# Kernel tuning notes

Hardware: AMD Instinct MI355X
Metric: run time of the kernel (lower is better)

Reference implementation:

```python
import jax, jax.numpy as jnp
import numpy as np

D_MODEL = 1024
MAX_ELEMENTS = 128


def setup_inputs() -> dict:
    key = jax.random.key(0)
    ks = jax.random.split(key, 12)
    B, S = 256, 128
    d, dq = D_MODEL, D_MODEL // 4
    inp = {
        "element_types": jax.random.randint(ks[0], (B, S), 0, 5, dtype=jnp.int64 if jax.config.jax_enable_x64 else jnp.int32),
        "element_indices": jax.random.randint(ks[1], (B, S), 0, MAX_ELEMENTS, dtype=jnp.int64 if jax.config.jax_enable_x64 else jnp.int32),
        "style_vectors": jax.random.normal(ks[2], (B, 5), dtype=jnp.float32),
        "page_captions": jax.random.normal(ks[3], (B, 768), dtype=jnp.float32),
        # learned parameters (torch Linear stored as [in, out] so y = x @ W + b)
        "type_emb": jax.random.normal(ks[4], (5, d), dtype=jnp.float32) * 0.02,
        "pos_emb": jax.random.normal(ks[5], (MAX_ELEMENTS, d), dtype=jnp.float32) * 0.02,
        "style_w1": jax.random.normal(ks[6], (5, dq), dtype=jnp.float32) * 0.02,
        "style_b1": jnp.zeros((dq,), dtype=jnp.float32),
        "style_w2": jax.random.normal(ks[7], (dq, d), dtype=jnp.float32) * 0.02,
        "style_b2": jnp.zeros((d,), dtype=jnp.float32),
        "text_w": jax.random.normal(ks[8], (768, d), dtype=jnp.float32) * 0.02,
        "text_b": jnp.zeros((d,), dtype=jnp.float32),
        "final_pos_emb": jax.random.normal(ks[9], (MAX_ELEMENTS, d), dtype=jnp.float32) * 0.02,
    }
    return inp


def reference(element_types, element_indices, style_vectors, page_captions,
              type_emb, pos_emb, style_w1, style_b1, style_w2, style_b2,
              text_w, text_b, final_pos_emb):
    B, S = element_types.shape
    # table gathers: [B, S, d]
    emb = type_emb[element_types] + pos_emb[element_indices]
    # per-batch style/text embeds computed ONCE (the torch loop recomputes them per step)
    style_embed = jnp.maximum(style_vectors @ style_w1 + style_b1, 0.0) @ style_w2 + style_b2  # [B, d]
    page_embed = page_captions @ text_w + text_b  # [B, d]
    # loop over i with mask (types[:, i] == 1) == broadcast masked add
    mask1 = (element_types == 1)[:, :, None]  # [B, S, 1]
    emb = emb + mask1 * (style_embed + page_embed)[:, None, :]
    # final positional encoding over positions 0..S-1
    emb = emb + final_pos_emb[:S][None, :, :]
    padding_mask = element_types == 0
    return emb, padding_mask
```

## Files before the change

kernel.cpp:

```cpp
#include <hip/hip_runtime.h>

#define D      1024
#define SEQ    128
#define BATCH  256
#define DQ     256
#define TEXTC  768

__global__ __launch_bounds__(256) void prep_kernel(
    const float* __restrict__ style_vectors,
    const float* __restrict__ page_captions,
    const float* __restrict__ style_w1,
    const float* __restrict__ style_b1,
    const float* __restrict__ style_b2,
    const float* __restrict__ text_b,
    float* __restrict__ act,
    float* __restrict__ comb)
{
    int i = blockIdx.x * 256 + threadIdx.x;
    int b = i >> 10;
    int k = i & 1023;
    float a;
    if (k < DQ) {
        float h = style_b1[k];
#pragma unroll
        for (int j = 0; j < 5; ++j)
            h = fmaf(style_vectors[b * 5 + j], style_w1[j * DQ + k], h);
        a = fmaxf(h, 0.0f);
    } else {
        a = page_captions[b * TEXTC + (k - DQ)];
    }
    act[i]  = a;
    comb[i] = style_b2[k] + text_b[k];
}

__global__ __launch_bounds__(256) void gemm_kernel(
    const float* __restrict__ act,
    const float* __restrict__ style_w2,
    const float* __restrict__ text_w,
    float* __restrict__ comb)
{
    __shared__ float As[16][64];
    __shared__ float Bs[16][64];

    const int m0  = blockIdx.x * 64;
    const int n0  = blockIdx.y * 64;
    const int k0  = blockIdx.z * 256;
    const int tid = threadIdx.x;
    const int tm  = tid >> 4;
    const int tn  = tid & 15;

    float acc[4][4] = {};

    for (int kc = 0; kc < 256; kc += 16) {
        {
            int m  = tid >> 2;
            int kq = tid & 3;
            float4 av = *(const float4*)&act[(m0 + m) * D + k0 + kc + kq * 4];
            As[kq * 4 + 0][m] = av.x;
            As[kq * 4 + 1][m] = av.y;
            As[kq * 4 + 2][m] = av.z;
            As[kq * 4 + 3][m] = av.w;
        }
        {
            int kk   = tid >> 4;
            int nq   = tid & 15;
            int krow = k0 + kc + kk;
            const float* Wrow = (krow < DQ) ? &style_w2[krow * D]
                                            : &text_w[(krow - DQ) * D];
            *(float4*)&Bs[kk][nq * 4] = *(const float4*)&Wrow[n0 + nq * 4];
        }
        __syncthreads();

#pragma unroll
        for (int kk = 0; kk < 16; ++kk) {
            float4 a4 = *(const float4*)&As[kk][tm * 4];
            float4 b4 = *(const float4*)&Bs[kk][tn * 4];
            float av[4] = {a4.x, a4.y, a4.z, a4.w};
            float bv[4] = {b4.x, b4.y, b4.z, b4.w};
#pragma unroll
            for (int ii = 0; ii < 4; ++ii)
#pragma unroll
                for (int jj = 0; jj < 4; ++jj)
                    acc[ii][jj] = fmaf(av[ii], bv[jj], acc[ii][jj]);
        }
        __syncthreads();
    }

#pragma unroll
    for (int ii = 0; ii < 4; ++ii) {
        int m = m0 + tm * 4 + ii;
#pragma unroll
        for (int jj = 0; jj < 4; ++jj)
            atomicAdd(&comb[m * D + n0 + tn * 4 + jj], acc[ii][jj]);
    }
}

__global__ __launch_bounds__(256) void scatter_kernel(
    const int* __restrict__ types,
    const int* __restrict__ indices,
    const float* __restrict__ type_emb,
    const float* __restrict__ pos_emb,
    const float* __restrict__ final_pos_emb,
    const float* __restrict__ comb,
    float* __restrict__ out_emb,
    float* __restrict__ out_mask)
{
    const int bs = blockIdx.x;
    const int b  = bs >> 7;
    const int s  = bs & 127;
    const int et = types[bs];
    const int ei = indices[bs];
    const int tid = threadIdx.x;

    const float4* te = (const float4*)&type_emb[et * D];
    const float4* pe = (const float4*)&pos_emb[ei * D];
    const float4* fe = (const float4*)&final_pos_emb[s * D];

    float4 t = te[tid];
    float4 p = pe[tid];
    float4 f = fe[tid];
    float4 v;
    v.x = t.x + p.x + f.x;
    v.y = t.y + p.y + f.y;
    v.z = t.z + p.z + f.z;
    v.w = t.w + p.w + f.w;
    if (et == 1) {
        float4 c = ((const float4*)&comb[b * D])[tid];
        v.x += c.x; v.y += c.y; v.z += c.z; v.w += c.w;
    }
    ((float4*)out_emb)[bs * 256 + tid] = v;

    if (tid == 0)
        out_mask[bs] = (et == 0) ? 1.0f : 0.0f;
}

extern "C" void kernel_launch(void* const* d_in, const int* in_sizes, int n_in,
                              void* d_out, int out_size, void* d_ws, size_t ws_size,
                              hipStream_t stream) {
    const int*   element_types   = (const int*)  d_in[0];
    const int*   element_indices = (const int*)  d_in[1];
    const float* style_vectors   = (const float*)d_in[2];
    const float* page_captions   = (const float*)d_in[3];
    const float* type_emb        = (const float*)d_in[4];
    const float* pos_emb         = (const float*)d_in[5];
    const float* style_w1        = (const float*)d_in[6];
    const float* style_b1        = (const float*)d_in[7];
    const float* style_w2        = (const float*)d_in[8];
    const float* style_b2        = (const float*)d_in[9];
    const float* text_w          = (const float*)d_in[10];
    const float* text_b          = (const float*)d_in[11];
    const float* final_pos_emb   = (const float*)d_in[12];

    float* act  = (float*)d_ws;
    float* comb = (float*)d_ws + BATCH * D;

    float* out_emb  = (float*)d_out;
    float* out_mask = (float*)d_out + BATCH * SEQ * D;

    prep_kernel<<<(BATCH * D) / 256, 256, 0, stream>>>(
        style_vectors, page_captions, style_w1, style_b1, style_b2, text_b,
        act, comb);

    gemm_kernel<<<dim3(BATCH / 64, D / 64, 4), 256, 0, stream>>>(
        act, style_w2, text_w, comb);

    scatter_kernel<<<BATCH * SEQ, 256, 0, stream>>>(
        element_types, element_indices, type_emb, pos_emb, final_pos_emb,
        comb, out_emb, out_mask);
}
```

Baseline: 214.2 us.

## Fuse prep into GEMM, replace atomics with split-K partials plus reduce, nontemporal stores

Computes the style MLP hidden layer and page-caption loads directly inside the GEMM's A-tile load, which removes the separate prep kernel and its act buffer. Each split-K slice now writes a partial result to its own buffer instead of using atomicAdd, and a small reduce kernel sums the four partials. Biases are folded into the z=0 slice. It also pads the shared-memory tiles and uses nontemporal stores for the large output write. The costs are an extra 4MB partial buffer round trip and an extra kernel launch.

```diff
diff --git a/kernel.cpp b/kernel.cpp
--- a/kernel.cpp
+++ b/kernel.cpp
@@ -6,93 +6,107 @@
 #define DQ     256
 #define TEXTC  768
 
-__global__ __launch_bounds__(256) void prep_kernel(
+typedef float f32x4 __attribute__((ext_vector_type(4)));
+
+__global__ __launch_bounds__(256) void gemm_fused(
     const float* __restrict__ style_vectors,
     const float* __restrict__ page_captions,
     const float* __restrict__ style_w1,
     const float* __restrict__ style_b1,
+    const float* __restrict__ style_w2,
     const float* __restrict__ style_b2,
+    const float* __restrict__ text_w,
     const float* __restrict__ text_b,
-    float* __restrict__ act,
-    float* __restrict__ comb)
+    float* __restrict__ part)
 {
-    int i = blockIdx.x * 256 + threadIdx.x;
-    int b = i >> 10;
-    int k = i & 1023;
-    float a;
-    if (k < DQ) {
-        float h = style_b1[k];
-#pragma unroll
-        for (int j = 0; j < 5; ++j)
-            h = fmaf(style_vectors[b * 5 + j], style_w1[j * DQ + k], h);
-        a = fmaxf(h, 0.0f);
-    } else {
-        a = page_captions[b * TEXTC + (k - DQ)];
-    }
-    act[i]  = a;
-    comb[i] = style_b2[k] + text_b[k];
-}
-
-__global__ __launch_bounds__(256) void gemm_kernel(
-    const float* __restrict__ act,
-    const float* __restrict__ style_w2,
-    const float* __restrict__ text_w,
-    float* __restrict__ comb)
-{
-    __shared__ float As[16][64];
-    __shared__ float Bs[16][64];
+    __shared__ float As[16][68];
+    __shared__ float Bs[16][68];
 
     const int m0  = blockIdx.x * 64;
     const int n0  = blockIdx.y * 64;
-    const int k0  = blockIdx.z * 256;
+    const int z   = blockIdx.z;
     const int tid = threadIdx.x;
     const int tm  = tid >> 4;
     const int tn  = tid & 15;
 
+    const int am = tid >> 2;
+    const int ak = (tid & 3) * 4;
+
+    float sv[5];
+    if (z == 0) {
+#pragma unroll
+        for (int j = 0; j < 5; ++j) sv[j] = style_vectors[(m0 + am) * 5 + j];
+    }
+
     float acc[4][4] = {};
 
     for (int kc = 0; kc < 256; kc += 16) {
-        {
-            int m  = tid >> 2;
-            int kq = tid & 3;
-            float4 av = *(const float4*)&act[(m0 + m) * D + k0 + kc + kq * 4];
-            As[kq * 4 + 0][m] = av.x;
-            As[kq * 4 + 1][m] = av.y;
-            As[kq * 4 + 2][m] = av.z;
-            As[kq * 4 + 3][m] = av.w;
+        if (z == 0) {
+            int k = kc + ak;
+#pragma unroll
+            for (int r = 0; r < 4; ++r) {
+                float h = style_b1[k + r];
+#pragma unroll
+                for (int j = 0; j < 5; ++j)
+                    h = fmaf(sv[j], style_w1[j * DQ + k + r], h);
+                As[ak + r][am] = fmaxf(h, 0.0f);
+            }
+        } else {
+            float4 av = *(const float4*)
+                &page_captions[(m0 + am) * TEXTC + (z * 256 - DQ) + kc + ak];
+            As[ak + 0][am] = av.x;
+            As[ak + 1][am] = av.y;
+            As[ak + 2][am] = av.z;
+            As[ak + 3][am] = av.w;
         }
         {
             int kk   = tid >> 4;
-            int nq   = tid & 15;
-            int krow = k0 + kc + kk;
-            const float* Wrow = (krow < DQ) ? &style_w2[krow * D]
-                                            : &text_w[(krow - DQ) * D];
-            *(float4*)&Bs[kk][nq * 4] = *(const float4*)&Wrow[n0 + nq * 4];
+            int nq   = (tid & 15) * 4;
+            int krow = z * 256 + kc + kk;
+            const float* Wrow = (z == 0) ? &style_w2[krow * D]
+                                         : &text_w[(krow - DQ) * D];
+            *(float4*)&Bs[kk][nq] = *(const float4*)&Wrow[n0 + nq];
         }
         __syncthreads();
 
 #pragma unroll
         for (int kk = 0; kk < 16; ++kk) {
-            float4 a4 = *(const float4*)&As[kk][tm * 4];
-            float4 b4 = *(const float4*)&Bs[kk][tn * 4];
-            float av[4] = {a4.x, a4.y, a4.z, a4.w};
-            float bv[4] = {b4.x, b4.y, b4.z, b4.w};
+            f32x4 a4 = *(const f32x4*)&As[kk][tm * 4];
+            f32x4 b4 = *(const f32x4*)&Bs[kk][tn * 4];
 #pragma unroll
             for (int ii = 0; ii < 4; ++ii)
 #pragma unroll
                 for (int jj = 0; jj < 4; ++jj)
-                    acc[ii][jj] = fmaf(av[ii], bv[jj], acc[ii][jj]);
+                    acc[ii][jj] = fmaf(a4[ii], b4[jj], acc[ii][jj]);
         }
         __syncthreads();
     }
 
+    float* dst = part + (size_t)z * BATCH * D;
+    const int n = n0 + tn * 4;
 #pragma unroll
     for (int ii = 0; ii < 4; ++ii) {
         int m = m0 + tm * 4 + ii;
-#pragma unroll
-        for (int jj = 0; jj < 4; ++jj)
-            atomicAdd(&comb[m * D + n0 + tn * 4 + jj], acc[ii][jj]);
+        f32x4 v = {acc[ii][0], acc[ii][1], acc[ii][2], acc[ii][3]};
+        if (z == 0) {
+            v[0] += style_b2[n + 0] + text_b[n + 0];
+            v[1] += style_b2[n + 1] + text_b[n + 1];
+            v[2] += style_b2[n + 2] + text_b[n + 2];
+            v[3] += style_b2[n + 3] + text_b[n + 3];
+        }
+        *(f32x4*)&dst[m * D + n] = v;
     }
+}
+
+__global__ __launch_bounds__(256) void reduce_part(
+    const float* __restrict__ part,
+    float* __restrict__ comb)
+{
+    const int i = blockIdx.x * 256 + threadIdx.x;
+    const f32x4* p = (const f32x4*)part;
+    const int Q = BATCH * D / 4;
+    f32x4 v = p[i] + p[i + Q] + p[i + 2 * Q] + p[i + 3 * Q];
+    ((f32x4*)comb)[i] = v;
 }
 
 __global__ __launch_bounds__(256) void scatter_kernel(
@@ -112,23 +126,14 @@
     const int ei = indices[bs];
     const int tid = threadIdx.x;
 
-    const float4* te = (const float4*)&type_emb[et * D];
-    const float4* pe = (const float4*)&pos_emb[ei * D];
-    const float4* fe = (const float4*)&final_pos_emb[s * D];
+    f32x4 t = ((const f32x4*)&type_emb[et * D])[tid];
+    f32x4 p = ((const f32x4*)&pos_emb[ei * D])[tid];
+    f32x4 f = ((const f32x4*)&final_pos_emb[s * D])[tid];
+    f32x4 v = t + p + f;
+    if (et == 1)
+        v = v + ((const f32x4*)&comb[b * D])[tid];
 
-    float4 t = te[tid];
-    float4 p = pe[tid];
-    float4 f = fe[tid];
-    float4 v;
-    v.x = t.x + p.x + f.x;
-    v.y = t.y + p.y + f.y;
-    v.z = t.z + p.z + f.z;
-    v.w = t.w + p.w + f.w;
-    if (et == 1) {
-        float4 c = ((const float4*)&comb[b * D])[tid];
-        v.x += c.x; v.y += c.y; v.z += c.z; v.w += c.w;
-    }
-    ((float4*)out_emb)[bs * 256 + tid] = v;
+    __builtin_nontemporal_store(v, &((f32x4*)out_emb)[bs * 256 + tid]);
 
     if (tid == 0)
         out_mask[bs] = (et == 0) ? 1.0f : 0.0f;
@@ -151,18 +156,17 @@
     const float* text_b          = (const float*)d_in[11];
     const float* final_pos_emb   = (const float*)d_in[12];
 
-    float* act  = (float*)d_ws;
-    float* comb = (float*)d_ws + BATCH * D;
+    float* part = (float*)d_ws;
+    float* comb = (float*)d_ws + 4 * BATCH * D;
 
     float* out_emb  = (float*)d_out;
     float* out_mask = (float*)d_out + BATCH * SEQ * D;
 
-    prep_kernel<<<(BATCH * D) / 256, 256, 0, stream>>>(
-        style_vectors, page_captions, style_w1, style_b1, style_b2, text_b,
-        act, comb);
+    gemm_fused<<<dim3(BATCH / 64, D / 64, 4), 256, 0, stream>>>(
+        style_vectors, page_captions, style_w1, style_b1,
+        style_w2, style_b2, text_w, text_b, part);
 
-    gemm_kernel<<<dim3(BATCH / 64, D / 64, 4), 256, 0, stream>>>(
-        act, style_w2, text_w, comb);
+    reduce_part<<<BATCH * D / 4 / 256, 256, 0, stream>>>(part, comb);
 
     scatter_kernel<<<BATCH * SEQ, 256, 0, stream>>>(
         element_types, element_indices, type_emb, pos_emb, final_pos_emb,
```

Measured after the change: 206.9 us. -3.4%, faster.
